# Kernel optimization log

Measured on AMD Instinct MI355X. Metric: run time of the kernel, lower is better.

## Reference

```python
import jax, jax.numpy as jnp
import numpy as np

B = 131072      # batch
H = 128         # hidden_size
NQ = 2          # num_qubits (forced: projector out = nq*4 viewed as (2,2,2) -> nq=2)
P = 2 * 4 ** NQ # LSTM proj_size = 32
D_IN = 1 + 8 * NQ  # 17 = 1 measurement + basis_dim
T = 16          # max_num_measurements


def setup_inputs() -> dict:
    key = jax.random.key(0)
    ks = iter(jax.random.split(key, 32))
    r = lambda *s: jax.random.normal(next(ks), s, dtype=jnp.float32)
    p = lambda *s: 0.05 * jax.random.normal(next(ks), s, dtype=jnp.float32)
    return {
        'measurement': r(B, 1),
        'basis_r': r(B, NQ, 2, 2),
        'basis_i': r(B, NQ, 2, 2),
        'rho': r(B, 2, 4, 4),
        'h0': r(B, H), 'c0': r(B, H),
        'Wih_cell': p(4 * H, D_IN), 'Whh_cell': p(4 * H, H),
        'bih_cell': p(4 * H), 'bhh_cell': p(4 * H),
        'Wp': p(NQ * 4, H), 'bp': p(NQ * 4),
        'Wih0': p(4 * H, D_IN), 'Whh0': p(4 * H, P), 'bih0': p(4 * H), 'bhh0': p(4 * H), 'Whr0': p(P, H),
        'Wih1': p(4 * H, P), 'Whh1': p(4 * H, P), 'bih1': p(4 * H), 'bhh1': p(4 * H), 'Whr1': p(P, H),
    }


def _lstm_proj(xs, Wih, Whh, bih, bhh, Whr):
    # torch nn.LSTM layer with proj_size: gates use projected h; gate order i,f,g,o
    Bn = xs.shape[1]
    h = jnp.zeros((Bn, Whr.shape[0]), xs.dtype)
    c = jnp.zeros((Bn, Whh.shape[0] // 4), xs.dtype)

    def step(carry, x):
        h, c = carry
        g = x @ Wih.T + h @ Whh.T + bih + bhh
        i, f, gg, o = jnp.split(g, 4, axis=-1)
        c = jax.nn.sigmoid(f) * c + jax.nn.sigmoid(i) * jnp.tanh(gg)
        hp = (jax.nn.sigmoid(o) * jnp.tanh(c)) @ Whr.T
        return (hp, c), hp

    _, ys = jax.lax.scan(step, (h, c), xs)
    return ys  # (T, B, P)


def reference(measurement, basis_r, basis_i, rho, h0, c0,
              Wih_cell, Whh_cell, bih_cell, bhh_cell, Wp, bp,
              Wih0, Whh0, bih0, bhh0, Whr0,
              Wih1, Whh1, bih1, bhh1, Whr1):
    Bn = measurement.shape[0]
    basis_vec = jnp.stack([basis_r, basis_i], axis=-1).reshape(Bn, NQ * 8)
    x0 = jnp.concatenate([measurement, basis_vec], axis=-1)  # (B, 17)
    # rho as complex tensor with per-qubit indices (row0,row1,col0,col1)
    rho_c = (rho[:, 0] + 1j * rho[:, 1]).astype(jnp.complex64).reshape(Bn, 2, 2, 2, 2)

    def step(carry, _):
        x, h, c = carry
        # LSTMCell (gate order i,f,g,o)
        g = x @ Wih_cell.T + h @ Whh_cell.T + bih_cell + bhh_cell
        i, f, gg, o = jnp.split(g, 4, axis=-1)
        c = jax.nn.sigmoid(f) * c + jax.nn.sigmoid(i) * jnp.tanh(gg)
        h = jax.nn.sigmoid(o) * jnp.tanh(c)
        # projector -> per-qubit complex 2-vectors
        v = (h @ Wp.T + bp).reshape(Bn, NQ, 2, 2)
        bv = (v[..., 0] + 1j * v[..., 1]).astype(jnp.complex64)  # (B, NQ, 2)
        # rank-1 measurement operators M_q = |v><v| / tr  (matches the 4 explicit entries)
        M = bv[..., :, None] * jnp.conj(bv[..., None, :])         # (B, NQ, 2, 2)
        tr = M[..., 0, 0] + M[..., 1, 1]
        M = M / tr[..., None, None]
        # measure: Tr[(M0 (x) M1) rho]
        meas = jnp.real(jnp.einsum('zac,zbd,zcdab->z', M[:, 0], M[:, 1], rho_c))
        nbv = jnp.stack([M.real, M.imag], axis=-1).reshape(Bn, NQ * 8)
        xn = jnp.concatenate([meas[:, None], nbv], axis=-1)
        return (xn, h, c), xn

    (_, _, _), xs = jax.lax.scan(step, (x0, h0, c0), None, length=T - 1)
    seq = jnp.concatenate([x0[None], xs], axis=0)  # (T, B, 17)
    y = _lstm_proj(seq, Wih0, Whh0, bih0, bhh0, Whr0)
    y = _lstm_proj(y, Wih1, Whh1, bih1, bhh1, Whr1)  # (T, B, 32)
    out = jnp.transpose(y, (1, 0, 2)).reshape(Bn, T, 2, 2 ** NQ, 2 ** NQ)
    return out
```

## Files before the change

### kernel.cpp

```cpp
#include <hip/hip_runtime.h>
#include <math.h>


constexpr int T_STEPS = 16;

__device__ __forceinline__ float fast_rcp(float x) { return __builtin_amdgcn_rcpf(x); }
__device__ __forceinline__ float sigmoid_f(float x) { return fast_rcp(1.f + __expf(-x)); }
__device__ __forceinline__ float tanh_f(float x) {
  return fmaf(-2.f, fast_rcp(1.f + __expf(2.f * x)), 1.f);
}

#define OFF_GENWX 0
#define OFF_GENWH 8704
#define OFF_L0WX  74240
#define OFF_L0WH  82944
#define OFF_L1WX  99328
#define OFF_L1WH  115712
#define OFF_GENB  132096
#define OFF_L0B   132608
#define OFF_L1B   133120

__global__ void reorder_w(const float* __restrict__ src, float* __restrict__ dst,
                          int K, int total) {
  int i = blockIdx.x * blockDim.x + threadIdx.x;
  if (i < total) {
    int g = i & 3;
    int n = (i >> 2) & 127;
    int k = i >> 9;
    dst[i] = src[(g * 128 + n) * K + k];
  }
}

__global__ void combine_bias(const float* __restrict__ a, const float* __restrict__ b,
                             float* __restrict__ dst) {
  int i = blockIdx.x * blockDim.x + threadIdx.x;
  if (i < 512) {
    int g = i & 3;
    int n = i >> 2;
    dst[i] = a[g * 128 + n] + b[g * 128 + n];
  }
}

template <int KX, int KH>
__device__ __forceinline__ void lstm_unit8(const float* __restrict__ shIn,
                                           const float* __restrict__ Wx,
                                           const float* __restrict__ shH,
                                           const float* __restrict__ Wh,
                                           const float* __restrict__ Bc,
                                           int n0, int e,
                                           float* __restrict__ cst,
                                           float* __restrict__ uout) {
  float acc[8][4];
#pragma unroll
  for (int j = 0; j < 8; ++j) {
#pragma unroll
    for (int g = 0; g < 4; ++g) acc[j][g] = Bc[(n0 + j) * 4 + g];
  }
#pragma unroll 2
  for (int k = 0; k < KX; ++k) {
    const float s = shIn[k * 64 + e];
    const float* w = Wx + (k * 128 + n0) * 4;
#pragma unroll
    for (int j = 0; j < 8; ++j)
#pragma unroll
      for (int g = 0; g < 4; ++g) acc[j][g] = fmaf(w[j * 4 + g], s, acc[j][g]);
  }
#pragma unroll 2
  for (int k = 0; k < KH; ++k) {
    const float s = shH[k * 64 + e];
    const float* w = Wh + (k * 128 + n0) * 4;
#pragma unroll
    for (int j = 0; j < 8; ++j)
#pragma unroll
      for (int g = 0; g < 4; ++g) acc[j][g] = fmaf(w[j * 4 + g], s, acc[j][g]);
  }
#pragma unroll
  for (int j = 0; j < 8; ++j) {
    float gi = sigmoid_f(acc[j][0]);
    float gf = sigmoid_f(acc[j][1]);
    float gg = tanh_f(acc[j][2]);
    float go = sigmoid_f(acc[j][3]);
    float cn = fmaf(gf, cst[j], gi * gg);
    cst[j] = cn;
    uout[j] = go * tanh_f(cn);
  }
}

__global__ __launch_bounds__(1024, 1) void lstm_fused(
    const float* __restrict__ measurement, const float* __restrict__ basis_r,
    const float* __restrict__ basis_i, const float* __restrict__ rho,
    const float* __restrict__ h0, const float* __restrict__ c0,
    const float* __restrict__ Wp, const float* __restrict__ bp,
    const float* __restrict__ Whr0, const float* __restrict__ Whr1,
    const float* __restrict__ ws, float* __restrict__ out) {
  __shared__ float sh_x[17 * 64];
  __shared__ float sh_genH[128 * 64];
  __shared__ float sh_l0H[32 * 64];
  __shared__ float sh_l1H[32 * 64];
  __shared__ float sh_u[128 * 64];
  __shared__ float sh_vp[16 * 64];
  __shared__ float sh_rho[32 * 65];

  const int tid = threadIdx.x;
  const int e = tid & 63;
  const int grp = __builtin_amdgcn_readfirstlane(tid >> 6);
  const int n0 = grp * 8;
  const int be = blockIdx.x * 64 + e;

  const float* genWx = ws + OFF_GENWX;
  const float* genWh = ws + OFF_GENWH;
  const float* l0Wx = ws + OFF_L0WX;
  const float* l0Wh = ws + OFF_L0WH;
  const float* l1Wx = ws + OFF_L1WX;
  const float* l1Wh = ws + OFF_L1WH;
  const float* genB = ws + OFF_GENB;
  const float* l0B = ws + OFF_L0B;
  const float* l1B = ws + OFF_L1B;

  for (int idx = tid; idx < 17 * 64; idx += 1024) {
    int k = idx >> 6, ee = idx & 63;
    int bee = blockIdx.x * 64 + ee;
    float val;
    if (k == 0) {
      val = measurement[bee];
    } else {
      int m = k - 1;
      const float* src = (m & 1) ? basis_i : basis_r;
      val = src[bee * 8 + (m >> 1)];
    }
    sh_x[idx] = val;
  }
  for (int idx = tid; idx < 128 * 64; idx += 1024) {
    int k = idx >> 6, ee = idx & 63;
    sh_genH[idx] = h0[(blockIdx.x * 64 + ee) * 128 + k];
  }
  for (int idx = tid; idx < 32 * 64; idx += 1024) {
    sh_l0H[idx] = 0.f;
    sh_l1H[idx] = 0.f;
  }
  for (int idx = tid; idx < 32 * 64; idx += 1024) {
    int ee = idx >> 5, i = idx & 31;
    sh_rho[i * 65 + ee] = rho[(blockIdx.x * 64 + ee) * 32 + i];
  }
  float cGen[8], cL0[8], cL1[8], uloc[8];
#pragma unroll
  for (int j = 0; j < 8; ++j) {
    cGen[j] = c0[be * 128 + n0 + j];
    cL0[j] = 0.f;
    cL1[j] = 0.f;
  }
  __syncthreads();

  for (int t = 0; t < T_STEPS; ++t) {
    lstm_unit8<17, 32>(sh_x, l0Wx, sh_l0H, l0Wh, l0B, n0, e, cL0, uloc);
#pragma unroll
    for (int j = 0; j < 8; ++j) sh_u[(n0 + j) * 64 + e] = uloc[j];
    __syncthreads();

    {
      float hp[2] = {0.f, 0.f};
      for (int k = 0; k < 128; ++k) {
        float uv = sh_u[k * 64 + e];
#pragma unroll
        for (int p = 0; p < 2; ++p) hp[p] = fmaf(Whr0[(grp * 2 + p) * 128 + k], uv, hp[p]);
      }
#pragma unroll
      for (int p = 0; p < 2; ++p) sh_l0H[(grp * 2 + p) * 64 + e] = hp[p];
    }
    __syncthreads();

    lstm_unit8<32, 32>(sh_l0H, l1Wx, sh_l1H, l1Wh, l1B, n0, e, cL1, uloc);
#pragma unroll
    for (int j = 0; j < 8; ++j) sh_u[(n0 + j) * 64 + e] = uloc[j];
    __syncthreads();

    {
      float hp[2] = {0.f, 0.f};
      for (int k = 0; k < 128; ++k) {
        float uv = sh_u[k * 64 + e];
#pragma unroll
        for (int p = 0; p < 2; ++p) hp[p] = fmaf(Whr1[(grp * 2 + p) * 128 + k], uv, hp[p]);
      }
#pragma unroll
      for (int p = 0; p < 2; ++p) sh_l1H[(grp * 2 + p) * 64 + e] = hp[p];
      *(float2*)(out + be * 512 + t * 32 + grp * 2) = make_float2(hp[0], hp[1]);
    }
    __syncthreads();

    if (t < T_STEPS - 1) {
      lstm_unit8<17, 128>(sh_x, genWx, sh_genH, genWh, genB, n0, e, cGen, uloc);
      __syncthreads();
#pragma unroll
      for (int j = 0; j < 8; ++j) sh_genH[(n0 + j) * 64 + e] = uloc[j];
      __syncthreads();

      {
        int r = grp & 7, half = grp >> 3;
        float acc = half ? 0.f : bp[r];
        int kb = half * 64;
        for (int k = 0; k < 64; ++k)
          acc = fmaf(Wp[r * 128 + kb + k], sh_genH[(kb + k) * 64 + e], acc);
        sh_vp[grp * 64 + e] = acc;
      }
      __syncthreads();

      if (tid < 64) {
        float v0[8];
#pragma unroll
        for (int r = 0; r < 8; ++r) v0[r] = sh_vp[r * 64 + e] + sh_vp[(r + 8) * 64 + e];
        float M[2][2][2][2];
#pragma unroll
        for (int q = 0; q < 2; ++q) {
          float b0r = v0[q * 4 + 0], b0i = v0[q * 4 + 1];
          float b1r = v0[q * 4 + 2], b1i = v0[q * 4 + 3];
          float m00 = b0r * b0r + b0i * b0i;
          float m11 = b1r * b1r + b1i * b1i;
          float m01r = b0r * b1r + b0i * b1i;
          float m01i = b0i * b1r - b0r * b1i;
          float inv = fast_rcp(m00 + m11);
          M[q][0][0][0] = m00 * inv;  M[q][0][0][1] = 0.f;
          M[q][0][1][0] = m01r * inv; M[q][0][1][1] = m01i * inv;
          M[q][1][0][0] = m01r * inv; M[q][1][0][1] = -m01i * inv;
          M[q][1][1][0] = m11 * inv;  M[q][1][1][1] = 0.f;
        }
        float meas = 0.f;
#pragma unroll
        for (int a = 0; a < 2; ++a)
#pragma unroll
          for (int cc = 0; cc < 2; ++cc) {
            float t0r = M[0][a][cc][0], t0i = M[0][a][cc][1];
#pragma unroll
            for (int bq = 0; bq < 2; ++bq)
#pragma unroll
              for (int d = 0; d < 2; ++d) {
                float t1r = M[1][bq][d][0], t1i = M[1][bq][d][1];
                float pr = t0r * t1r - t0i * t1i;
                float pi = t0r * t1i + t0i * t1r;
                int rrow = cc * 2 + d, rcol = a * 2 + bq;
                float zr = sh_rho[(rrow * 4 + rcol) * 65 + e];
                float zi = sh_rho[(16 + rrow * 4 + rcol) * 65 + e];
                meas += pr * zr - pi * zi;
              }
          }
        sh_x[0 * 64 + e] = meas;
#pragma unroll
        for (int q = 0; q < 2; ++q)
#pragma unroll
          for (int i = 0; i < 2; ++i)
#pragma unroll
            for (int j = 0; j < 2; ++j) {
              sh_x[(1 + q * 8 + i * 4 + j * 2 + 0) * 64 + e] = M[q][i][j][0];
              sh_x[(1 + q * 8 + i * 4 + j * 2 + 1) * 64 + e] = M[q][i][j][1];
            }
      }
      __syncthreads();
    }
  }
}

extern "C" void kernel_launch(void* const* d_in, const int* in_sizes, int n_in,
                              void* d_out, int out_size, void* d_ws, size_t ws_size,
                              hipStream_t stream) {
  const float* measurement = (const float*)d_in[0];
  const float* basis_r = (const float*)d_in[1];
  const float* basis_i = (const float*)d_in[2];
  const float* rho = (const float*)d_in[3];
  const float* h0 = (const float*)d_in[4];
  const float* c0 = (const float*)d_in[5];
  const float* Wih_cell = (const float*)d_in[6];
  const float* Whh_cell = (const float*)d_in[7];
  const float* bih_cell = (const float*)d_in[8];
  const float* bhh_cell = (const float*)d_in[9];
  const float* Wp = (const float*)d_in[10];
  const float* bp = (const float*)d_in[11];
  const float* Wih0 = (const float*)d_in[12];
  const float* Whh0 = (const float*)d_in[13];
  const float* bih0 = (const float*)d_in[14];
  const float* bhh0 = (const float*)d_in[15];
  const float* Whr0 = (const float*)d_in[16];
  const float* Wih1 = (const float*)d_in[17];
  const float* Whh1 = (const float*)d_in[18];
  const float* bih1 = (const float*)d_in[19];
  const float* bhh1 = (const float*)d_in[20];
  const float* Whr1 = (const float*)d_in[21];
  float* out = (float*)d_out;
  float* ws = (float*)d_ws;

  const int B = in_sizes[0];

  reorder_w<<<(512 * 17 + 255) / 256, 256, 0, stream>>>(Wih_cell, ws + OFF_GENWX, 17, 512 * 17);
  reorder_w<<<(512 * 128 + 255) / 256, 256, 0, stream>>>(Whh_cell, ws + OFF_GENWH, 128, 512 * 128);
  reorder_w<<<(512 * 17 + 255) / 256, 256, 0, stream>>>(Wih0, ws + OFF_L0WX, 17, 512 * 17);
  reorder_w<<<(512 * 32 + 255) / 256, 256, 0, stream>>>(Whh0, ws + OFF_L0WH, 32, 512 * 32);
  reorder_w<<<(512 * 32 + 255) / 256, 256, 0, stream>>>(Wih1, ws + OFF_L1WX, 32, 512 * 32);
  reorder_w<<<(512 * 32 + 255) / 256, 256, 0, stream>>>(Whh1, ws + OFF_L1WH, 32, 512 * 32);
  combine_bias<<<2, 256, 0, stream>>>(bih_cell, bhh_cell, ws + OFF_GENB);
  combine_bias<<<2, 256, 0, stream>>>(bih0, bhh0, ws + OFF_L0B);
  combine_bias<<<2, 256, 0, stream>>>(bih1, bhh1, ws + OFF_L1B);

  lstm_fused<<<B / 64, 1024, 0, stream>>>(measurement, basis_r, basis_i, rho, h0, c0,
                                          Wp, bp, Whr0, Whr1, ws, out);
}
```

Measured before the change: 9.688 ms.

## Halve projection scratch LDS to fit two 1024-thread blocks per CU

The 128x64 `sh_u` staging buffer is replaced by a 64x64 buffer. The Whr projection is now done in two halves: the first eight wave groups write their gate outputs, everyone accumulates, then the other eight groups overwrite the buffer and everyone accumulates the rest. `sh_vp` is aliased onto this buffer and launch bounds ask for two blocks per CU. The aim is to cut LDS per block enough for a second resident block, giving more latency hiding. The cost is extra barriers per step and a tighter register budget that may cause spills.

```diff
diff --git a/kernel.cpp b/kernel.cpp
--- a/kernel.cpp
+++ b/kernel.cpp
@@ -86,7 +86,7 @@
   }
 }
 
-__global__ __launch_bounds__(1024, 1) void lstm_fused(
+__global__ __launch_bounds__(1024, 2) void lstm_fused(
     const float* __restrict__ measurement, const float* __restrict__ basis_r,
     const float* __restrict__ basis_i, const float* __restrict__ rho,
     const float* __restrict__ h0, const float* __restrict__ c0,
@@ -97,9 +97,10 @@
   __shared__ float sh_genH[128 * 64];
   __shared__ float sh_l0H[32 * 64];
   __shared__ float sh_l1H[32 * 64];
-  __shared__ float sh_u[128 * 64];
-  __shared__ float sh_vp[16 * 64];
+  __shared__ float sh_uh[64 * 64];
   __shared__ float sh_rho[32 * 65];
+
+  float* const sh_vp = sh_uh;
 
   const int tid = threadIdx.x;
   const int e = tid & 63;
@@ -153,16 +154,30 @@
 
   for (int t = 0; t < T_STEPS; ++t) {
     lstm_unit8<17, 32>(sh_x, l0Wx, sh_l0H, l0Wh, l0B, n0, e, cL0, uloc);
-#pragma unroll
-    for (int j = 0; j < 8; ++j) sh_u[(n0 + j) * 64 + e] = uloc[j];
-    __syncthreads();
 
     {
+      if (grp < 8) {
+#pragma unroll
+        for (int j = 0; j < 8; ++j) sh_uh[(n0 + j) * 64 + e] = uloc[j];
+      }
+      __syncthreads();
       float hp[2] = {0.f, 0.f};
-      for (int k = 0; k < 128; ++k) {
-        float uv = sh_u[k * 64 + e];
+      for (int k = 0; k < 64; ++k) {
+        float uv = sh_uh[k * 64 + e];
 #pragma unroll
         for (int p = 0; p < 2; ++p) hp[p] = fmaf(Whr0[(grp * 2 + p) * 128 + k], uv, hp[p]);
+      }
+      __syncthreads();
+      if (grp >= 8) {
+#pragma unroll
+        for (int j = 0; j < 8; ++j) sh_uh[(n0 - 64 + j) * 64 + e] = uloc[j];
+      }
+      __syncthreads();
+      for (int k = 0; k < 64; ++k) {
+        float uv = sh_uh[k * 64 + e];
+#pragma unroll
+        for (int p = 0; p < 2; ++p)
+          hp[p] = fmaf(Whr0[(grp * 2 + p) * 128 + 64 + k], uv, hp[p]);
       }
 #pragma unroll
       for (int p = 0; p < 2; ++p) sh_l0H[(grp * 2 + p) * 64 + e] = hp[p];
@@ -170,16 +185,30 @@
     __syncthreads();
 
     lstm_unit8<32, 32>(sh_l0H, l1Wx, sh_l1H, l1Wh, l1B, n0, e, cL1, uloc);
-#pragma unroll
-    for (int j = 0; j < 8; ++j) sh_u[(n0 + j) * 64 + e] = uloc[j];
-    __syncthreads();
 
     {
+      if (grp < 8) {
+#pragma unroll
+        for (int j = 0; j < 8; ++j) sh_uh[(n0 + j) * 64 + e] = uloc[j];
+      }
+      __syncthreads();
       float hp[2] = {0.f, 0.f};
-      for (int k = 0; k < 128; ++k) {
-        float uv = sh_u[k * 64 + e];
+      for (int k = 0; k < 64; ++k) {
+        float uv = sh_uh[k * 64 + e];
 #pragma unroll
         for (int p = 0; p < 2; ++p) hp[p] = fmaf(Whr1[(grp * 2 + p) * 128 + k], uv, hp[p]);
+      }
+      __syncthreads();
+      if (grp >= 8) {
+#pragma unroll
+        for (int j = 0; j < 8; ++j) sh_uh[(n0 - 64 + j) * 64 + e] = uloc[j];
+      }
+      __syncthreads();
+      for (int k = 0; k < 64; ++k) {
+        float uv = sh_uh[k * 64 + e];
+#pragma unroll
+        for (int p = 0; p < 2; ++p)
+          hp[p] = fmaf(Whr1[(grp * 2 + p) * 128 + 64 + k], uv, hp[p]);
       }
 #pragma unroll
       for (int p = 0; p < 2; ++p) sh_l1H[(grp * 2 + p) * 64 + e] = hp[p];
```

After: 9.956 ms. 2.8% more time.
